# Performance work log

Measured on AMD Instinct MI355X. Metric: run time of the kernel, lower is better.

## Reference

```python
import jax, jax.numpy as jnp
import numpy as np

N_NODES = 50000
N_EDGES = 25000  # hyperedges
NNZ = 400000     # incidence pairs


def _segment_mean(x, idx, num_segments):
    s = jax.ops.segment_sum(x, idx, num_segments=num_segments)
    cnt = jax.ops.segment_sum(jnp.ones((x.shape[0], 1), x.dtype), idx, num_segments=num_segments)
    return s / jnp.maximum(cnt, 1.0)


def _unigcn_conv(X, W, vertex, edges, degE, degV):
    # X: [N, Cin] -> [N, Cout]
    X = X @ W                                   # linear (no bias)
    Xve = X[vertex]                             # gather per incidence [nnz, C]
    Xe = _segment_mean(Xve, edges, N_EDGES)     # first_aggregate='mean' over hyperedges
    Xe = Xe * degE                              # [M,1] scale
    Xev = Xe[edges]                             # gather back [nnz, C]
    Xv = jax.ops.segment_sum(Xev, vertex, num_segments=N_NODES)
    return Xv * degV                            # [N,1] scale


def setup_inputs() -> dict:
    key = jax.random.key(0)
    ks = jax.random.split(key, 8)
    nfeat, nhid_total, nclass = 512, 512, 40
    def glorot(k, fan_in, fan_out):
        std = np.sqrt(6.0 / (fan_in + fan_out))
        return jax.random.uniform(k, (fan_in, fan_out), jnp.float32, -std, std)
    return {
        "X": jax.random.normal(ks[0], (N_NODES, nfeat), jnp.float32),
        "vertex": jax.random.randint(ks[1], (NNZ,), 0, N_NODES, jnp.int32),
        "edges": jax.random.randint(ks[2], (NNZ,), 0, N_EDGES, jnp.int32),
        "W1": glorot(ks[3], nfeat, nhid_total),
        "W2": glorot(ks[4], nhid_total, nhid_total),
        "Wout": glorot(ks[5], nhid_total, nclass),
        "degE": jax.random.uniform(ks[6], (N_EDGES, 1), jnp.float32, 0.1, 1.0),
        "degV": jax.random.uniform(ks[7], (N_NODES, 1), jnp.float32, 0.1, 1.0),
    }


def reference(X, vertex, edges, W1, W2, Wout, degE, degV):
    # dropout layers are identity at eval (rates = 0)
    X = jax.nn.relu(_unigcn_conv(X, W1, vertex, edges, degE, degV))
    X = jax.nn.relu(_unigcn_conv(X, W2, vertex, edges, degE, degV))
    X = _unigcn_conv(X, Wout, vertex, edges, degE, degV)
    return jax.nn.log_softmax(X, axis=1)
```

## Files before the change

kernel.cpp:

```cpp
#include <hip/hip_runtime.h>

#define N_NODES 50000
#define N_EDGES_C 25000
#define NNZ_C 400000
#define SCHUNK 2048

typedef __bf16 bf16;
typedef __bf16 bf16x8 __attribute__((ext_vector_type(8)));
typedef __bf16 bf16x4 __attribute__((ext_vector_type(4)));
typedef float f32x4 __attribute__((ext_vector_type(4)));

typedef __attribute__((address_space(1))) const void as1_cvoid;
typedef __attribute__((address_space(3))) void as3_void;

__device__ __forceinline__ void gload_lds16(const bf16* g, bf16* l) {
  __builtin_amdgcn_global_load_lds((as1_cvoid*)g, (as3_void*)l, 16, 0, 0);
}

__global__ void hist_kernel(const int* __restrict__ vtx, const int* __restrict__ edg,
                            int* __restrict__ cntV, int* __restrict__ cntE, int nnz) {
  int i = blockIdx.x * blockDim.x + threadIdx.x;
  if (i < nnz) {
    atomicAdd(&cntV[vtx[i]], 1);
    atomicAdd(&cntE[edg[i]], 1);
  }
}

__global__ void scan_part(const int* __restrict__ cnt, int* __restrict__ part, int n) {
  __shared__ int red[256];
  const int b = blockIdx.x, t = threadIdx.x;
  const int base = b * SCHUNK + t * 8;
  int s = 0;
#pragma unroll
  for (int q = 0; q < 8; ++q) {
    int i = base + q;
    if (i < n) s += cnt[i];
  }
  red[t] = s;
  __syncthreads();
  for (int d = 128; d > 0; d >>= 1) {
    if (t < d) red[t] += red[t + d];
    __syncthreads();
  }
  if (t == 0) part[b] = red[0];
}

__global__ void scan_mid(int* __restrict__ part, int* __restrict__ off, int nparts, int n) {
  const int lane = threadIdx.x;
  int orig = (lane < nparts) ? part[lane] : 0;
  int v = orig;
  for (int o = 1; o < 64; o <<= 1) {
    int x = __shfl_up(v, o);
    if (lane >= o) v += x;
  }
  if (lane < nparts) part[lane] = v - orig;
  if (lane == 63) off[n] = v;
}

__global__ void scan_final(const int* __restrict__ cnt, const int* __restrict__ part,
                           int* __restrict__ off, int n) {
  __shared__ int tsum[256];
  const int b = blockIdx.x, t = threadIdx.x;
  const int base = b * SCHUNK + t * 8;
  int loc[8];
  int s = 0;
#pragma unroll
  for (int q = 0; q < 8; ++q) {
    int i = base + q;
    loc[q] = (i < n) ? cnt[i] : 0;
    s += loc[q];
  }
  tsum[t] = s;
  __syncthreads();
  for (int d = 1; d < 256; d <<= 1) {
    int x = (t >= d) ? tsum[t - d] : 0;
    __syncthreads();
    tsum[t] += x;
    __syncthreads();
  }
  int run = part[b] + ((t > 0) ? tsum[t - 1] : 0);
#pragma unroll
  for (int q = 0; q < 8; ++q) {
    int i = base + q;
    if (i < n) off[i] = run;
    run += loc[q];
  }
}

__global__ void scatter_kernel(const int* __restrict__ vtx, const int* __restrict__ edg,
                               const int* __restrict__ eoff, const int* __restrict__ voff,
                               int* __restrict__ curE, int* __restrict__ curV,
                               int* __restrict__ evtx, int* __restrict__ vedg, int nnz) {
  int i = blockIdx.x * blockDim.x + threadIdx.x;
  if (i < nnz) {
    int e = edg[i], v = vtx[i];
    int p = atomicAdd(&curE[e], 1);
    evtx[eoff[e] + p] = v;
    int q = atomicAdd(&curV[v], 1);
    vedg[voff[v] + q] = e;
  }
}

__global__ void convert_f2b(const float* __restrict__ in, bf16* __restrict__ out, size_t n) {
  size_t i = ((size_t)blockIdx.x * blockDim.x + threadIdx.x) * 4;
  if (i >= n) return;
  float4 v = *(const float4*)(in + i);
  bf16x4 o;
  o[0] = (bf16)v.x; o[1] = (bf16)v.y; o[2] = (bf16)v.z; o[3] = (bf16)v.w;
  *(bf16x4*)(out + i) = o;
}

__global__ void transpose_w(const float* __restrict__ W, bf16* __restrict__ Wt,
                            int K, int N, int NtRows) {
  int idx = blockIdx.x * blockDim.x + threadIdx.x;
  int total = NtRows * K;
  if (idx >= total) return;
  int n = idx / K;
  int k = idx - n * K;
  Wt[idx] = (n < N) ? (bf16)W[(size_t)k * N + n] : (bf16)0.0f;
}

template <int BF16OUT>
__global__ __launch_bounds__(256) void gemm_bf16_kernel(
    const bf16* __restrict__ A, const bf16* __restrict__ B,
    float* __restrict__ Cf, bf16* __restrict__ Cb, int M, int K, int ldC, int Nstore) {
  __shared__ bf16 Al[2][128][64];
  __shared__ bf16 Bl[2][128][64];
  const int t = threadIdx.x;
  const int m0 = blockIdx.x * 128;
  const int n0 = blockIdx.y * 128;
  const int w = t >> 6, lane = t & 63;
  const int wr = w >> 1, wc = w & 1;
  const int lr = lane & 15;
  const int ls = lane >> 4;

  f32x4 acc[4][4];
#pragma unroll
  for (int m = 0; m < 4; ++m)
#pragma unroll
    for (int n = 0; n < 4; ++n) acc[m][n] = (f32x4){0.f, 0.f, 0.f, 0.f};

  const int srow8 = lane >> 3;
  const int scol = ((lane & 7) ^ srow8) << 3;

  const bf16* Abase = A + (size_t)m0 * K;
  const bf16* Bbase = B + (size_t)n0 * K;

#define STAGE(tile, bsel)                                                        \
  {                                                                              \
    const int kk_ = (tile) * 64;                                                 \
    _Pragma("unroll")                                                            \
    for (int q = 0; q < 4; ++q) {                                                \
      const int row = w * 32 + q * 8 + srow8;                                    \
      gload_lds16(Abase + (size_t)row * K + kk_ + scol, &Al[bsel][w*32+q*8][0]); \
      gload_lds16(Bbase + (size_t)row * K + kk_ + scol, &Bl[bsel][w*32+q*8][0]); \
    }                                                                            \
  }

  const int NT = K >> 6;
  STAGE(0, 0);
  for (int tt = 0; tt < NT; ++tt) {
    const int cur = tt & 1;
    if (tt + 1 < NT) {
      STAGE(tt + 1, cur ^ 1);
      asm volatile("s_waitcnt vmcnt(8)" ::: "memory");
    } else {
      asm volatile("s_waitcnt vmcnt(0)" ::: "memory");
    }
    __builtin_amdgcn_s_barrier();
    __builtin_amdgcn_s_setprio(1);
#pragma unroll
    for (int ks = 0; ks < 2; ++ks) {
      bf16x8 af[4], bfr[4];
#pragma unroll
      for (int m = 0; m < 4; ++m) {
        const int R = wr * 64 + m * 16 + lr;
        af[m] = *(const bf16x8*)(&Al[cur][R][((ks * 4 + ls) ^ (lr & 7)) << 3]);
      }
#pragma unroll
      for (int n = 0; n < 4; ++n) {
        const int R = wc * 64 + n * 16 + lr;
        bfr[n] = *(const bf16x8*)(&Bl[cur][R][((ks * 4 + ls) ^ (lr & 7)) << 3]);
      }
#pragma unroll
      for (int m = 0; m < 4; ++m)
#pragma unroll
        for (int n = 0; n < 4; ++n)
          acc[m][n] = __builtin_amdgcn_mfma_f32_16x16x32_bf16(af[m], bfr[n], acc[m][n], 0, 0, 0);
    }
    __builtin_amdgcn_s_setprio(0);
    __builtin_amdgcn_s_barrier();
  }
#undef STAGE

  const int cr = (lane >> 4) << 2;
  const int cc = lane & 15;
#pragma unroll
  for (int m = 0; m < 4; ++m) {
#pragma unroll
    for (int n = 0; n < 4; ++n) {
      int gc = n0 + wc * 64 + n * 16 + cc;
      if (gc >= Nstore) continue;
#pragma unroll
      for (int i = 0; i < 4; ++i) {
        int gr = m0 + wr * 64 + m * 16 + cr + i;
        if (gr < M) {
          if (BF16OUT) Cb[(size_t)gr * ldC + gc] = (bf16)acc[m][n][i];
          else         Cf[(size_t)gr * ldC + gc] = acc[m][n][i];
        }
      }
    }
  }
}

__global__ __launch_bounds__(256) void edge_agg_w(
    const bf16* __restrict__ Y, const int* __restrict__ eoff, const int* __restrict__ evtx,
    const float* __restrict__ degE, bf16* __restrict__ Xe, int nE) {
  const int wv = (blockIdx.x * 256 + threadIdx.x) >> 6;
  if (wv >= nE) return;
  const int lane = threadIdx.x & 63;
  const int beg = eoff[wv], end = eoff[wv + 1];
  const int cnt = end - beg;
  const float scale = (cnt > 0) ? degE[wv] / (float)cnt : 0.f;
  float acc[8] = {0.f, 0.f, 0.f, 0.f, 0.f, 0.f, 0.f, 0.f};
  for (int base = beg; base < end; base += 64) {
    const int nb = min(64, end - base);
    int myidx = (lane < nb) ? evtx[base + lane] : 0;
    int j = 0;
    for (; j + 1 < nb; j += 2) {
      const int i0 = __shfl(myidx, j);
      const int i1 = __shfl(myidx, j + 1);
      bf16x8 v0 = *(const bf16x8*)(Y + (size_t)i0 * 512 + lane * 8);
      bf16x8 v1 = *(const bf16x8*)(Y + (size_t)i1 * 512 + lane * 8);
#pragma unroll
      for (int q = 0; q < 8; ++q) acc[q] += (float)v0[q] + (float)v1[q];
    }
    if (j < nb) {
      const int i0 = __shfl(myidx, j);
      bf16x8 v0 = *(const bf16x8*)(Y + (size_t)i0 * 512 + lane * 8);
#pragma unroll
      for (int q = 0; q < 8; ++q) acc[q] += (float)v0[q];
    }
  }
  bf16x8 o;
#pragma unroll
  for (int q = 0; q < 8; ++q) o[q] = (bf16)(acc[q] * scale);
  *(bf16x8*)(Xe + (size_t)wv * 512 + lane * 8) = o;
}

__global__ __launch_bounds__(256) void vtx_agg_w(
    const bf16* __restrict__ Xe, const int* __restrict__ voff, const int* __restrict__ vedg,
    const float* __restrict__ degV, bf16* __restrict__ outB, int nV) {
  const int wv = (blockIdx.x * 256 + threadIdx.x) >> 6;
  if (wv >= nV) return;
  const int lane = threadIdx.x & 63;
  const int beg = voff[wv], end = voff[wv + 1];
  const float dv = degV[wv];
  float acc[8] = {0.f, 0.f, 0.f, 0.f, 0.f, 0.f, 0.f, 0.f};
  for (int base = beg; base < end; base += 64) {
    const int nb = min(64, end - base);
    int myidx = (lane < nb) ? vedg[base + lane] : 0;
    int j = 0;
    for (; j + 1 < nb; j += 2) {
      const int i0 = __shfl(myidx, j);
      const int i1 = __shfl(myidx, j + 1);
      bf16x8 v0 = *(const bf16x8*)(Xe + (size_t)i0 * 512 + lane * 8);
      bf16x8 v1 = *(const bf16x8*)(Xe + (size_t)i1 * 512 + lane * 8);
#pragma unroll
      for (int q = 0; q < 8; ++q) acc[q] += (float)v0[q] + (float)v1[q];
    }
    if (j < nb) {
      const int i0 = __shfl(myidx, j);
      bf16x8 v0 = *(const bf16x8*)(Xe + (size_t)i0 * 512 + lane * 8);
#pragma unroll
      for (int q = 0; q < 8; ++q) acc[q] += (float)v0[q];
    }
  }
  bf16x8 o;
#pragma unroll
  for (int q = 0; q < 8; ++q) o[q] = (bf16)fmaxf(acc[q] * dv, 0.f);
  *(bf16x8*)(outB + (size_t)wv * 512 + lane * 8) = o;
}

__global__ __launch_bounds__(256) void edge_agg40_w(
    const float* __restrict__ Y, const int* __restrict__ eoff, const int* __restrict__ evtx,
    const float* __restrict__ degE, float* __restrict__ Xe, int nE) {
  const int wv = (blockIdx.x * 256 + threadIdx.x) >> 6;
  if (wv >= nE) return;
  const int lane = threadIdx.x & 63;
  const int beg = eoff[wv], end = eoff[wv + 1];
  const int cnt = end - beg;
  const float scale = (cnt > 0) ? degE[wv] / (float)cnt : 0.f;
  float a0 = 0.f;
  for (int base = beg; base < end; base += 64) {
    const int nb = min(64, end - base);
    int myidx = (lane < nb) ? evtx[base + lane] : 0;
    int j = 0;
    for (; j + 3 < nb; j += 4) {
      const int i0 = __shfl(myidx, j);
      const int i1 = __shfl(myidx, j + 1);
      const int i2 = __shfl(myidx, j + 2);
      const int i3 = __shfl(myidx, j + 3);
      if (lane < 40) {
        float x0 = Y[(size_t)i0 * 40 + lane];
        float x1 = Y[(size_t)i1 * 40 + lane];
        float x2 = Y[(size_t)i2 * 40 + lane];
        float x3 = Y[(size_t)i3 * 40 + lane];
        a0 += (x0 + x1) + (x2 + x3);
      }
    }
    for (; j < nb; ++j) {
      const int i0 = __shfl(myidx, j);
      if (lane < 40) a0 += Y[(size_t)i0 * 40 + lane];
    }
  }
  if (lane < 40) Xe[(size_t)wv * 40 + lane] = a0 * scale;
}

__global__ __launch_bounds__(256) void vtx_agg_lsm(
    const float* __restrict__ Xe, const int* __restrict__ voff, const int* __restrict__ vedg,
    const float* __restrict__ degV, float* __restrict__ out, int nV) {
  const int wv = (blockIdx.x * 256 + threadIdx.x) >> 6;
  if (wv >= nV) return;
  const int lane = threadIdx.x & 63;
  const int beg = voff[wv], end = voff[wv + 1];
  const float dv = degV[wv];
  float a0 = 0.f;
  for (int base = beg; base < end; base += 64) {
    const int nb = min(64, end - base);
    int myidx = (lane < nb) ? vedg[base + lane] : 0;
    int j = 0;
    for (; j + 3 < nb; j += 4) {
      const int i0 = __shfl(myidx, j);
      const int i1 = __shfl(myidx, j + 1);
      const int i2 = __shfl(myidx, j + 2);
      const int i3 = __shfl(myidx, j + 3);
      if (lane < 40) {
        float x0 = Xe[(size_t)i0 * 40 + lane];
        float x1 = Xe[(size_t)i1 * 40 + lane];
        float x2 = Xe[(size_t)i2 * 40 + lane];
        float x3 = Xe[(size_t)i3 * 40 + lane];
        a0 += (x0 + x1) + (x2 + x3);
      }
    }
    for (; j < nb; ++j) {
      const int i0 = __shfl(myidx, j);
      if (lane < 40) a0 += Xe[(size_t)i0 * 40 + lane];
    }
  }
  a0 *= dv;
  float val = (lane < 40) ? a0 : -3.4e38f;
  float m = val;
#pragma unroll
  for (int o = 32; o > 0; o >>= 1) m = fmaxf(m, __shfl_xor(m, o));
  float ex = (lane < 40) ? expf(val - m) : 0.f;
  float s = ex;
#pragma unroll
  for (int o = 32; o > 0; o >>= 1) s += __shfl_xor(s, o);
  float ls = logf(s);
  if (lane < 40) out[(size_t)wv * 40 + lane] = val - m - ls;
}

extern "C" void kernel_launch(void* const* d_in, const int* in_sizes, int n_in,
                              void* d_out, int out_size, void* d_ws, size_t ws_size,
                              hipStream_t stream) {
  (void)in_sizes; (void)n_in; (void)out_size; (void)ws_size;
  const float* X = (const float*)d_in[0];
  const int* vertex = (const int*)d_in[1];
  const int* edges = (const int*)d_in[2];
  const float* W1 = (const float*)d_in[3];
  const float* W2 = (const float*)d_in[4];
  const float* Wout = (const float*)d_in[5];
  const float* degE = (const float*)d_in[6];
  const float* degV = (const float*)d_in[7];
  float* out = (float*)d_out;

  char* ws = (char*)d_ws;
  size_t off = 0;
  auto alloc = [&](size_t bytes) -> void* {
    void* p = ws + off;
    off += (bytes + 255) & ~(size_t)255;
    return p;
  };
  bf16* Xb  = (bf16*)alloc((size_t)N_NODES * 512 * sizeof(bf16));
  bf16* Yb  = (bf16*)alloc((size_t)N_NODES * 512 * sizeof(bf16));
  bf16* XeB = (bf16*)alloc((size_t)N_EDGES_C * 512 * sizeof(bf16));
  float* Y40  = (float*)alloc((size_t)N_NODES * 40 * sizeof(float));
  float* Xe40 = (float*)alloc((size_t)N_EDGES_C * 40 * sizeof(float));
  bf16* Wt  = (bf16*)alloc((size_t)512 * 512 * sizeof(bf16));
  int* eoff = (int*)alloc((N_EDGES_C + 1) * sizeof(int));
  int* voff = (int*)alloc((N_NODES + 1) * sizeof(int));
  int* evtx = (int*)alloc((size_t)NNZ_C * sizeof(int));
  int* vedg = (int*)alloc((size_t)NNZ_C * sizeof(int));
  int* cntE = (int*)alloc(N_EDGES_C * sizeof(int));
  int* cntV = (int*)alloc(N_NODES * sizeof(int));
  int* curE = (int*)alloc(N_EDGES_C * sizeof(int));
  int* curV = (int*)alloc(N_NODES * sizeof(int));
  int* partE = (int*)alloc(64 * sizeof(int));
  int* partV = (int*)alloc(64 * sizeof(int));

  hipMemsetAsync(cntE, 0, N_EDGES_C * sizeof(int), stream);
  hipMemsetAsync(cntV, 0, N_NODES * sizeof(int), stream);
  hipMemsetAsync(curE, 0, N_EDGES_C * sizeof(int), stream);
  hipMemsetAsync(curV, 0, N_NODES * sizeof(int), stream);

  hist_kernel<<<(NNZ_C + 255) / 256, 256, 0, stream>>>(vertex, edges, cntV, cntE, NNZ_C);

  const int nbE = (N_EDGES_C + SCHUNK - 1) / SCHUNK;
  const int nbV = (N_NODES + SCHUNK - 1) / SCHUNK;
  scan_part<<<nbE, 256, 0, stream>>>(cntE, partE, N_EDGES_C);
  scan_mid<<<1, 64, 0, stream>>>(partE, eoff, nbE, N_EDGES_C);
  scan_final<<<nbE, 256, 0, stream>>>(cntE, partE, eoff, N_EDGES_C);
  scan_part<<<nbV, 256, 0, stream>>>(cntV, partV, N_NODES);
  scan_mid<<<1, 64, 0, stream>>>(partV, voff, nbV, N_NODES);
  scan_final<<<nbV, 256, 0, stream>>>(cntV, partV, voff, N_NODES);

  scatter_kernel<<<(NNZ_C + 255) / 256, 256, 0, stream>>>(vertex, edges, eoff, voff,
                                                          curE, curV, evtx, vedg, NNZ_C);

  convert_f2b<<<(N_NODES * 512 / 4 + 255) / 256, 256, 0, stream>>>(X, Xb, (size_t)N_NODES * 512);

  const int MB = (N_NODES + 127) / 128;

  transpose_w<<<(512 * 512 + 255) / 256, 256, 0, stream>>>(W1, Wt, 512, 512, 512);
  {
    dim3 g(MB, 4);
    gemm_bf16_kernel<1><<<g, 256, 0, stream>>>(Xb, Wt, nullptr, Yb, N_NODES, 512, 512, 512);
  }
  edge_agg_w<<<(N_EDGES_C + 3) / 4, 256, 0, stream>>>(Yb, eoff, evtx, degE, XeB, N_EDGES_C);
  vtx_agg_w<<<(N_NODES + 3) / 4, 256, 0, stream>>>(XeB, voff, vedg, degV, Xb, N_NODES);

  transpose_w<<<(512 * 512 + 255) / 256, 256, 0, stream>>>(W2, Wt, 512, 512, 512);
  {
    dim3 g(MB, 4);
    gemm_bf16_kernel<1><<<g, 256, 0, stream>>>(Xb, Wt, nullptr, Yb, N_NODES, 512, 512, 512);
  }
  edge_agg_w<<<(N_EDGES_C + 3) / 4, 256, 0, stream>>>(Yb, eoff, evtx, degE, XeB, N_EDGES_C);
  vtx_agg_w<<<(N_NODES + 3) / 4, 256, 0, stream>>>(XeB, voff, vedg, degV, Xb, N_NODES);

  transpose_w<<<(128 * 512 + 255) / 256, 256, 0, stream>>>(Wout, Wt, 512, 40, 128);
  {
    dim3 g(MB, 1);
    gemm_bf16_kernel<0><<<g, 256, 0, stream>>>(Xb, Wt, Y40, nullptr, N_NODES, 512, 40, 40);
  }
  edge_agg40_w<<<(N_EDGES_C + 3) / 4, 256, 0, stream>>>(Y40, eoff, evtx, degE, Xe40, N_EDGES_C);
  vtx_agg_lsm<<<(N_NODES + 3) / 4, 256, 0, stream>>>(Xe40, voff, vedg, degV, out, N_NODES);
}
```

Before: 543.7 us.

## Fuse fp32-to-bf16 conversion into first GEMM and batch prep/scan launches

The first GEMM now loads fp32 X directly into registers, converts it to bf16 and writes it into LDS, removing the separate conversion kernel and its intermediate buffer traffic. The weight transposes are merged into one prep kernel with separate buffers, the edge and vertex scans are merged into combined kernels, and the counter memsets collapse into one. The GEMM grid is reordered so column tiles of the same row block run adjacently, improving A reuse in cache. The fp32 A path doubles A load bytes inside the GEMM and uses a register-staged load instead of direct-to-LDS loads.

```diff
diff --git a/kernel.cpp b/kernel.cpp
--- a/kernel.cpp
+++ b/kernel.cpp
@@ -26,9 +26,15 @@
   }
 }
 
-__global__ void scan_part(const int* __restrict__ cnt, int* __restrict__ part, int n) {
+__global__ void scan_part2(const int* __restrict__ cntE, const int* __restrict__ cntV,
+                           int* __restrict__ partE, int* __restrict__ partV,
+                           int nbE) {
   __shared__ int red[256];
-  const int b = blockIdx.x, t = threadIdx.x;
+  const int t = threadIdx.x;
+  const int isV = (blockIdx.x >= nbE);
+  const int b = isV ? (blockIdx.x - nbE) : blockIdx.x;
+  const int* cnt = isV ? cntV : cntE;
+  const int n = isV ? N_NODES : N_EDGES_C;
   const int base = b * SCHUNK + t * 8;
   int s = 0;
 #pragma unroll
@@ -42,25 +48,39 @@
     if (t < d) red[t] += red[t + d];
     __syncthreads();
   }
-  if (t == 0) part[b] = red[0];
-}
-
-__global__ void scan_mid(int* __restrict__ part, int* __restrict__ off, int nparts, int n) {
-  const int lane = threadIdx.x;
-  int orig = (lane < nparts) ? part[lane] : 0;
+  if (t == 0) (isV ? partV : partE)[b] = red[0];
+}
+
+__global__ void scan_mid2(int* __restrict__ partE, int* __restrict__ partV,
+                          int* __restrict__ eoff, int* __restrict__ voff,
+                          int nbE, int nbV) {
+  const int wv = threadIdx.x >> 6;
+  const int lane = threadIdx.x & 63;
+  int* part = wv ? partV : partE;
+  int* off = wv ? voff : eoff;
+  const int np = wv ? nbV : nbE;
+  const int n = wv ? N_NODES : N_EDGES_C;
+  int orig = (lane < np) ? part[lane] : 0;
   int v = orig;
   for (int o = 1; o < 64; o <<= 1) {
     int x = __shfl_up(v, o);
     if (lane >= o) v += x;
   }
-  if (lane < nparts) part[lane] = v - orig;
+  if (lane < np) part[lane] = v - orig;
   if (lane == 63) off[n] = v;
 }
 
-__global__ void scan_final(const int* __restrict__ cnt, const int* __restrict__ part,
-                           int* __restrict__ off, int n) {
+__global__ void scan_final2(const int* __restrict__ cntE, const int* __restrict__ cntV,
+                            const int* __restrict__ partE, const int* __restrict__ partV,
+                            int* __restrict__ eoff, int* __restrict__ voff, int nbE) {
   __shared__ int tsum[256];
-  const int b = blockIdx.x, t = threadIdx.x;
+  const int t = threadIdx.x;
+  const int isV = (blockIdx.x >= nbE);
+  const int b = isV ? (blockIdx.x - nbE) : blockIdx.x;
+  const int* cnt = isV ? cntV : cntE;
+  const int* part = isV ? partV : partE;
+  int* off = isV ? voff : eoff;
+  const int n = isV ? N_NODES : N_EDGES_C;
   const int base = b * SCHUNK + t * 8;
   int loc[8];
   int s = 0;
@@ -101,23 +121,25 @@
   }
 }
 
-__global__ void convert_f2b(const float* __restrict__ in, bf16* __restrict__ out, size_t n) {
-  size_t i = ((size_t)blockIdx.x * blockDim.x + threadIdx.x) * 4;
-  if (i >= n) return;
-  float4 v = *(const float4*)(in + i);
-  bf16x4 o;
-  o[0] = (bf16)v.x; o[1] = (bf16)v.y; o[2] = (bf16)v.z; o[3] = (bf16)v.w;
-  *(bf16x4*)(out + i) = o;
-}
-
-__global__ void transpose_w(const float* __restrict__ W, bf16* __restrict__ Wt,
-                            int K, int N, int NtRows) {
-  int idx = blockIdx.x * blockDim.x + threadIdx.x;
-  int total = NtRows * K;
-  if (idx >= total) return;
-  int n = idx / K;
-  int k = idx - n * K;
-  Wt[idx] = (n < N) ? (bf16)W[(size_t)k * N + n] : (bf16)0.0f;
+__global__ void prep_kernel(const float* __restrict__ W1, const float* __restrict__ W2,
+                            const float* __restrict__ Wout,
+                            bf16* __restrict__ Wt1, bf16* __restrict__ Wt2,
+                            bf16* __restrict__ Wt3) {
+  int b = blockIdx.x;
+  const int t = threadIdx.x;
+  if (b < 1024) {
+    int idx = b * 256 + t;
+    int n = idx >> 9, k = idx & 511;
+    Wt1[idx] = (bf16)W1[(size_t)k * 512 + n];
+  } else if (b < 2048) {
+    int idx = (b - 1024) * 256 + t;
+    int n = idx >> 9, k = idx & 511;
+    Wt2[idx] = (bf16)W2[(size_t)k * 512 + n];
+  } else {
+    int idx = (b - 2048) * 256 + t;
+    int n = idx >> 9, k = idx & 511;
+    Wt3[idx] = (n < 40) ? (bf16)Wout[(size_t)k * 40 + n] : (bf16)0.0f;
+  }
 }
 
 template <int BF16OUT>
@@ -127,8 +149,8 @@
   __shared__ bf16 Al[2][128][64];
   __shared__ bf16 Bl[2][128][64];
   const int t = threadIdx.x;
-  const int m0 = blockIdx.x * 128;
-  const int n0 = blockIdx.y * 128;
+  const int n0 = blockIdx.x * 128;
+  const int m0 = blockIdx.y * 128;
   const int w = t >> 6, lane = t & 63;
   const int wr = w >> 1, wc = w & 1;
   const int lr = lane & 15;
@@ -208,6 +230,127 @@
           if (BF16OUT) Cb[(size_t)gr * ldC + gc] = (bf16)acc[m][n][i];
           else         Cf[(size_t)gr * ldC + gc] = acc[m][n][i];
         }
+      }
+    }
+  }
+}
+
+__global__ __launch_bounds__(256) void gemm_af32_kernel(
+    const float* __restrict__ Af, const bf16* __restrict__ B,
+    bf16* __restrict__ Cb, int M, int K, int ldC) {
+  __shared__ bf16 Al[2][128][64];
+  __shared__ bf16 Bl[2][128][64];
+  const int t = threadIdx.x;
+  const int n0 = blockIdx.x * 128;
+  const int m0 = blockIdx.y * 128;
+  const int w = t >> 6, lane = t & 63;
+  const int wr = w >> 1, wc = w & 1;
+  const int lr = lane & 15;
+  const int ls = lane >> 4;
+
+  f32x4 acc[4][4];
+#pragma unroll
+  for (int m = 0; m < 4; ++m)
+#pragma unroll
+    for (int n = 0; n < 4; ++n) acc[m][n] = (f32x4){0.f, 0.f, 0.f, 0.f};
+
+  const int cc_ = t & 7;
+  const int r0 = t >> 3;
+  const int physc = cc_ ^ (r0 & 7);
+  const int srow8 = lane >> 3;
+  const int scol = ((lane & 7) ^ srow8) << 3;
+  const bf16* Bbase = B + (size_t)n0 * K;
+
+  float4 fa[4], fb[4];
+
+#define AISSUE(tile)                                                   \
+  { const int kk_ = (tile) * 64;                                       \
+    _Pragma("unroll") for (int q = 0; q < 4; ++q) {                    \
+      int grow = m0 + r0 + 32 * q; if (grow > M - 1) grow = M - 1;     \
+      const float* p = Af + (size_t)grow * K + kk_ + cc_ * 8;          \
+      fa[q] = *(const float4*)p;                                       \
+      fb[q] = *(const float4*)(p + 4); } }
+
+#define AWRITE(bsel)                                                   \
+  { _Pragma("unroll") for (int q = 0; q < 4; ++q) {                    \
+      bf16x8 cv;                                                       \
+      cv[0] = (bf16)fa[q].x; cv[1] = (bf16)fa[q].y;                    \
+      cv[2] = (bf16)fa[q].z; cv[3] = (bf16)fa[q].w;                    \
+      cv[4] = (bf16)fb[q].x; cv[5] = (bf16)fb[q].y;                    \
+      cv[6] = (bf16)fb[q].z; cv[7] = (bf16)fb[q].w;                    \
+      *(bf16x8*)(&Al[bsel][r0 + 32 * q][physc * 8]) = cv; } }
+
+#define BSTAGE(tile, bsel)                                                       \
+  { const int kk_ = (tile) * 64;                                                 \
+    _Pragma("unroll") for (int q = 0; q < 4; ++q) {                              \
+      const int row = w * 32 + q * 8 + srow8;                                    \
+      gload_lds16(Bbase + (size_t)row * K + kk_ + scol, &Bl[bsel][w*32+q*8][0]); \
+    } }
+
+  const int NT = K >> 6;
+  AISSUE(0);
+  __builtin_amdgcn_sched_barrier(0);
+  BSTAGE(0, 0);
+  __builtin_amdgcn_sched_barrier(0);
+  asm volatile("s_waitcnt vmcnt(4)" ::: "memory");
+  AWRITE(0);
+  asm volatile("s_waitcnt lgkmcnt(0)" ::: "memory");
+
+  for (int tt = 0; tt < NT; ++tt) {
+    const int cur = tt & 1;
+    if (tt + 1 < NT) {
+      AISSUE(tt + 1);
+      __builtin_amdgcn_sched_barrier(0);
+      BSTAGE(tt + 1, cur ^ 1);
+      __builtin_amdgcn_sched_barrier(0);
+      asm volatile("s_waitcnt vmcnt(12)" ::: "memory");
+    } else {
+      asm volatile("s_waitcnt vmcnt(0)" ::: "memory");
+    }
+    __builtin_amdgcn_s_barrier();
+    __builtin_amdgcn_s_setprio(1);
+#pragma unroll
+    for (int ks = 0; ks < 2; ++ks) {
+      bf16x8 af[4], bfr[4];
+#pragma unroll
+      for (int m = 0; m < 4; ++m) {
+        const int R = wr * 64 + m * 16 + lr;
+        af[m] = *(const bf16x8*)(&Al[cur][R][((ks * 4 + ls) ^ (lr & 7)) << 3]);
+      }
+#pragma unroll
+      for (int n = 0; n < 4; ++n) {
+        const int R = wc * 64 + n * 16 + lr;
+        bfr[n] = *(const bf16x8*)(&Bl[cur][R][((ks * 4 + ls) ^ (lr & 7)) << 3]);
+      }
+#pragma unroll
+      for (int m = 0; m < 4; ++m)
+#pragma unroll
+        for (int n = 0; n < 4; ++n)
+          acc[m][n] = __builtin_amdgcn_mfma_f32_16x16x32_bf16(af[m], bfr[n], acc[m][n], 0, 0, 0);
+    }
+    __builtin_amdgcn_s_setprio(0);
+    if (tt + 1 < NT) {
+      asm volatile("s_waitcnt vmcnt(4)" ::: "memory");
+      AWRITE(cur ^ 1);
+      asm volatile("s_waitcnt lgkmcnt(0)" ::: "memory");
+    }
+    __builtin_amdgcn_s_barrier();
+  }
+#undef AISSUE
+#undef AWRITE
+#undef BSTAGE
+
+  const int cr = (lane >> 4) << 2;
+  const int cc = lane & 15;
+#pragma unroll
+  for (int m = 0; m < 4; ++m) {
+#pragma unroll
+    for (int n = 0; n < 4; ++n) {
+      int gc = n0 + wc * 64 + n * 16 + cc;
+#pragma unroll
+      for (int i = 0; i < 4; ++i) {
+        int gr = m0 + wr * 64 + m * 16 + cr + i;
+        if (gr < M) Cb[(size_t)gr * ldC + gc] = (bf16)acc[m][n][i];
       }
     }
   }
@@ -387,61 +530,55 @@
   bf16* XeB = (bf16*)alloc((size_t)N_EDGES_C * 512 * sizeof(bf16));
   float* Y40  = (float*)alloc((size_t)N_NODES * 40 * sizeof(float));
   float* Xe40 = (float*)alloc((size_t)N_EDGES_C * 40 * sizeof(float));
-  bf16* Wt  = (bf16*)alloc((size_t)512 * 512 * sizeof(bf16));
+  bf16* Wt1 = (bf16*)alloc((size_t)512 * 512 * sizeof(bf16));
+  bf16* Wt2 = (bf16*)alloc((size_t)512 * 512 * sizeof(bf16));
+  bf16* Wt3 = (bf16*)alloc((size_t)128 * 512 * sizeof(bf16));
   int* eoff = (int*)alloc((N_EDGES_C + 1) * sizeof(int));
   int* voff = (int*)alloc((N_NODES + 1) * sizeof(int));
   int* evtx = (int*)alloc((size_t)NNZ_C * sizeof(int));
   int* vedg = (int*)alloc((size_t)NNZ_C * sizeof(int));
-  int* cntE = (int*)alloc(N_EDGES_C * sizeof(int));
-  int* cntV = (int*)alloc(N_NODES * sizeof(int));
-  int* curE = (int*)alloc(N_EDGES_C * sizeof(int));
-  int* curV = (int*)alloc(N_NODES * sizeof(int));
+  int* cnts = (int*)alloc((size_t)(2 * (N_EDGES_C + N_NODES)) * sizeof(int));
+  int* cntE = cnts;
+  int* cntV = cnts + N_EDGES_C;
+  int* curE = cnts + N_EDGES_C + N_NODES;
+  int* curV = cnts + 2 * N_EDGES_C + N_NODES;
   int* partE = (int*)alloc(64 * sizeof(int));
   int* partV = (int*)alloc(64 * sizeof(int));
 
-  hipMemsetAsync(cntE, 0, N_EDGES_C * sizeof(int), stream);
-  hipMemsetAsync(cntV, 0, N_NODES * sizeof(int), stream);
-  hipMemsetAsync(curE, 0, N_EDGES_C * sizeof(int), stream);
-  hipMemsetAsync(curV, 0, N_NODES * sizeof(int), stream);
+  hipMemsetAsync(cnts, 0, (size_t)(2 * (N_EDGES_C + N_NODES)) * sizeof(int), stream);
+
+  prep_kernel<<<2304, 256, 0, stream>>>(W1, W2, Wout, Wt1, Wt2, Wt3);
 
   hist_kernel<<<(NNZ_C + 255) / 256, 256, 0, stream>>>(vertex, edges, cntV, cntE, NNZ_C);
 
   const int nbE = (N_EDGES_C + SCHUNK - 1) / SCHUNK;
   const int nbV = (N_NODES + SCHUNK - 1) / SCHUNK;
-  scan_part<<<nbE, 256, 0, stream>>>(cntE, partE, N_EDGES_C);
-  scan_mid<<<1, 64, 0, stream>>>(partE, eoff, nbE, N_EDGES_C);
-  scan_final<<<nbE, 256, 0, stream>>>(cntE, partE, eoff, N_EDGES_C);
-  scan_part<<<nbV, 256, 0, stream>>>(cntV, partV, N_NODES);
-  scan_mid<<<1, 64, 0, stream>>>(partV, voff, nbV, N_NODES);
-  scan_final<<<nbV, 256, 0, stream>>>(cntV, partV, voff, N_NODES);
+  scan_part2<<<nbE + nbV, 256, 0, stream>>>(cntE, cntV, partE, partV, nbE);
+  scan_mid2<<<1, 128, 0, stream>>>(partE, partV, eoff, voff, nbE, nbV);
+  scan_final2<<<nbE + nbV, 256, 0, stream>>>(cntE, cntV, partE, partV, eoff, voff, nbE);
 
   scatter_kernel<<<(NNZ_C + 255) / 256, 256, 0, stream>>>(vertex, edges, eoff, voff,
                                                           curE, curV, evtx, vedg, NNZ_C);
 
-  convert_f2b<<<(N_NODES * 512 / 4 + 255) / 256, 256, 0, stream>>>(X, Xb, (size_t)N_NODES * 512);
-
   const int MB = (N_NODES + 127) / 128;
 
-  transpose_w<<<(512 * 512 + 255) / 256, 256, 0, stream>>>(W1, Wt, 512, 512, 512);
   {
-    dim3 g(MB, 4);
-    gemm_bf16_kernel<1><<<g, 256, 0, stream>>>(Xb, Wt, nullptr, Yb, N_NODES, 512, 512, 512);
+    dim3 g(4, MB);
+    gemm_af32_kernel<<<g, 256, 0, stream>>>(X, Wt1, Yb, N_NODES, 512, 512);
   }
   edge_agg_w<<<(N_EDGES_C + 3) / 4, 256, 0, stream>>>(Yb, eoff, evtx, degE, XeB, N_EDGES_C);
   vtx_agg_w<<<(N_NODES + 3) / 4, 256, 0, stream>>>(XeB, voff, vedg, degV, Xb, N_NODES);
 
-  transpose_w<<<(512 * 512 + 255) / 256, 256, 0, stream>>>(W2, Wt, 512, 512, 512);
   {
-    dim3 g(MB, 4);
-    gemm_bf16_kernel<1><<<g, 256, 0, stream>>>(Xb, Wt, nullptr, Yb, N_NODES, 512, 512, 512);
+    dim3 g(4, MB);
+    gemm_bf16_kernel<1><<<g, 256, 0, stream>>>(Xb, Wt2, nullptr, Yb, N_NODES, 512, 512, 512);
   }
   edge_agg_w<<<(N_EDGES_C + 3) / 4, 256, 0, stream>>>(Yb, eoff, evtx, degE, XeB, N_EDGES_C);
   vtx_agg_w<<<(N_NODES + 3) / 4, 256, 0, stream>>>(XeB, voff, vedg, degV, Xb, N_NODES);
 
-  transpose_w<<<(128 * 512 + 255) / 256, 256, 0, stream>>>(Wout, Wt, 512, 40, 128);
   {
-    dim3 g(MB, 1);
-    gemm_bf16_kernel<0><<<g, 256, 0, stream>>>(Xb, Wt, Y40, nullptr, N_NODES, 512, 40, 40);
+    dim3 g(1, MB);
+    gemm_bf16_kernel<0><<<g, 256, 0, stream>>>(Xb, Wt3, Y40, nullptr, N_NODES, 512, 40, 40);
   }
   edge_agg40_w<<<(N_EDGES_C + 3) / 4, 256, 0, stream>>>(Y40, eoff, evtx, degE, Xe40, N_EDGES_C);
   vtx_agg_lsm<<<(N_NODES + 3) / 4, 256, 0, stream>>>(Xe40, voff, vedg, degV, out, N_NODES);
```

Result: faster. 519.0 us (-4.6%).
